# Performance work log

Hardware: AMD Instinct MI355X
Metric: run time of the kernel (lower is better)

Reference implementation:

```python
import jax, jax.numpy as jnp
import numpy as np

N_NODES = 100000
EPS = 1e-5


def _layernorm(x, g, b):
    # per-node layer norm over feature dim
    mu = jnp.mean(x, axis=-1, keepdims=True)
    var = jnp.mean(jnp.square(x - mu), axis=-1, keepdims=True)
    return (x - mu) * jax.lax.rsqrt(var + EPS) * g + b


def _gcn_conv(x, W, b, src, dst, n_nodes):
    # GCNConv: xW, then symmetric-normalized aggregation with self-loops.
    xw = x @ W  # [N, out]
    ones = jnp.ones(src.shape[0], dtype=x.dtype)
    deg = jax.ops.segment_sum(ones, dst, num_segments=n_nodes) + 1.0  # +1 self loop
    dinv = jax.lax.rsqrt(deg)  # [N]
    norm = dinv[src] * dinv[dst]  # [E]
    msg = xw[src] * norm[:, None]  # [E, out]  <- dominant memory traffic
    agg = jax.ops.segment_sum(msg, dst, num_segments=n_nodes)
    agg = agg + xw * (dinv * dinv)[:, None]  # self-loop contribution
    return agg + b


def setup_inputs() -> dict:
    key = jax.random.key(0)
    ks = jax.random.split(key, 16)
    in_c, hid, out_c = 128, 64, 32
    E = 1_600_000
    d = {}
    d['x'] = jax.random.normal(ks[0], (N_NODES, in_c), dtype=jnp.float32)
    d['edge_index'] = jax.random.randint(ks[1], (2, E), 0, N_NODES, dtype=jnp.int64)

    def lin(k, fi, fo):
        s = 1.0 / np.sqrt(fi)
        k1, k2 = jax.random.split(k)
        return (jax.random.uniform(k1, (fi, fo), jnp.float32, -s, s),
                jax.random.uniform(k2, (fo,), jnp.float32, -s, s))

    d['W1'], d['b1'] = lin(ks[2], in_c, hid)
    d['g1'], d['be1'] = jnp.ones((hid,), jnp.float32), jnp.zeros((hid,), jnp.float32)
    d['W2'], d['b2'] = lin(ks[3], hid, 2 * hid)
    d['g2'], d['be2'] = jnp.ones((2 * hid,), jnp.float32), jnp.zeros((2 * hid,), jnp.float32)
    d['W3'], d['b3'] = lin(ks[4], 2 * hid, hid)
    d['g3'], d['be3'] = jnp.ones((hid,), jnp.float32), jnp.zeros((hid,), jnp.float32)
    d['lw1'], d['lb1'] = lin(ks[5], hid, hid // 2)
    d['g4'], d['be4'] = jnp.ones((hid // 2,), jnp.float32), jnp.zeros((hid // 2,), jnp.float32)
    d['lw2'], d['lb2'] = lin(ks[6], hid // 2, out_c)
    return d


def reference(x, edge_index, W1, b1, g1, be1, W2, b2, g2, be2, W3, b3, g3, be3,
              lw1, lb1, g4, be4, lw2, lb2):
    src, dst = edge_index[0], edge_index[1]
    h = _gcn_conv(x, W1, b1, src, dst, N_NODES)
    h = jax.nn.elu(_layernorm(h, g1, be1))
    h = _gcn_conv(h, W2, b2, src, dst, N_NODES)
    h = jax.nn.elu(_layernorm(h, g2, be2))
    h = _gcn_conv(h, W3, b3, src, dst, N_NODES)
    h = jax.nn.elu(_layernorm(h, g3, be3))
    h = h @ lw1 + lb1
    h = jax.nn.elu(_layernorm(h, g4, be4))
    return h @ lw2 + lb2
```

## Files before the change

kernel.cpp:

```cpp
#include <hip/hip_runtime.h>
#include <math.h>

#define N_NODES 100000
#define LN_EPS 1e-5f
#define NBUCK ((N_NODES + 255) / 256)
#define EPB 8192

typedef __attribute__((ext_vector_type(8))) short bf16x8;
typedef __attribute__((ext_vector_type(4))) float f32x4;

__device__ __forceinline__ unsigned short f2bf(float f) {
    unsigned int u = __float_as_uint(f);
    return (unsigned short)((u + 0x7FFFu + ((u >> 16) & 1u)) >> 16);
}
__device__ __forceinline__ float bf2f(unsigned short u) {
    return __uint_as_float(((unsigned int)u) << 16);
}


__global__ void count_edges(const int* __restrict__ dst, int* __restrict__ counts, int E) {
    __shared__ int hist[NBUCK];
    for (int b = threadIdx.x; b < NBUCK; b += 512) hist[b] = 0;
    __syncthreads();
    int e0 = blockIdx.x * EPB;
#pragma unroll 4
    for (int i = 0; i < EPB / 512; ++i) {
        int e = e0 + i * 512 + (int)threadIdx.x;
        if (e < E) atomicAdd(&hist[((unsigned)dst[e]) >> 8], 1);
    }
    __syncthreads();
    for (int b = threadIdx.x; b < NBUCK; b += 512)
        counts[blockIdx.x * NBUCK + b] = hist[b];
}

__global__ void scan_pos(const int* __restrict__ counts, int* __restrict__ pos,
                         int* __restrict__ tot, int nblk) {
    __shared__ int s[512];
    int b = blockIdx.x, i = threadIdx.x;
    int v = (i < nblk) ? counts[i * NBUCK + b] : 0;
    s[i] = v;
    __syncthreads();
    for (int off = 1; off < 512; off <<= 1) {
        int t = (i >= off) ? s[i - off] : 0;
        __syncthreads();
        s[i] += t;
        __syncthreads();
    }
    if (i < nblk) pos[i * NBUCK + b] = s[i] - v;
    if (i == 511) tot[b] = s[511];
}

__global__ void scan_base(const int* __restrict__ tot, int* __restrict__ base, int E) {
    __shared__ int s[512];
    int i = threadIdx.x;
    int v = (i < NBUCK) ? tot[i] : 0;
    s[i] = v;
    __syncthreads();
    for (int off = 1; off < 512; off <<= 1) {
        int t = (i >= off) ? s[i - off] : 0;
        __syncthreads();
        s[i] += t;
        __syncthreads();
    }
    if (i < NBUCK) base[i] = s[i] - v;
    if (i == 0) base[NBUCK] = E;
}

__global__ void place_edges(const int* __restrict__ src, const int* __restrict__ dst,
                            const int* __restrict__ pos, const int* __restrict__ base,
                            unsigned* __restrict__ bucket, int E) {
    __shared__ int lcur[NBUCK];
    for (int b = threadIdx.x; b < NBUCK; b += 512)
        lcur[b] = pos[blockIdx.x * NBUCK + b] + base[b];
    __syncthreads();
    int e0 = blockIdx.x * EPB;
#pragma unroll 4
    for (int i = 0; i < EPB / 512; ++i) {
        int e = e0 + i * 512 + (int)threadIdx.x;
        if (e < E) {
            unsigned d = (unsigned)dst[e];
            unsigned s = (unsigned)src[e];
            int p = atomicAdd(&lcur[d >> 8], 1);
            bucket[p] = ((d & 255u) << 24) | s;
        }
    }
}

__global__ void build_csr_node(const unsigned* __restrict__ bucket, const int* __restrict__ base,
                               int* __restrict__ offsets, float* __restrict__ dinv,
                               int* __restrict__ csr, int E) {
    __shared__ int hist[256];
    __shared__ int cur[256];
    int b = blockIdx.x, t = threadIdx.x;
    int r0 = b << 8;
    hist[t] = 0;
    __syncthreads();
    int s0 = base[b], s1 = base[b + 1];
    for (int e = s0 + t; e < s1; e += 256)
        atomicAdd(&hist[bucket[e] >> 24], 1);
    __syncthreads();
    int deg = hist[t];
    for (int off = 1; off < 256; off <<= 1) {
        int tv = (t >= off) ? hist[t - off] : 0;
        __syncthreads();
        hist[t] += tv;
        __syncthreads();
    }
    int excl = hist[t] - deg;
    int node = r0 + t;
    if (node < N_NODES) {
        offsets[node] = s0 + excl;
        dinv[node] = rsqrtf((float)deg + 1.f);
        cur[t] = s0 + excl;
    }
    if (node == N_NODES - 1) offsets[N_NODES] = E;
    __syncthreads();
    for (int e = s0 + t; e < s1; e += 256) {
        unsigned u = bucket[e];
        int p = atomicAdd(&cur[u >> 24], 1);
        csr[p] = (int)(u & 0xFFFFFFu);
    }
}

template <int K, int OUT, bool LN, bool BIAS, bool AF32, bool OF32, bool SCALED>
__launch_bounds__(256)
__global__ void mfma_gemm(const void* __restrict__ Xv, const float* __restrict__ W,
                          const float* __restrict__ bias, const float* __restrict__ gamma,
                          const float* __restrict__ beta, void* __restrict__ Yv, int n,
                          const float* __restrict__ dinvp) {
    constexpr int T  = OUT / 16;
    constexpr int KP = K + 8;

    __shared__ __align__(16) unsigned short sWT[OUT * KP];
    for (int i = threadIdx.x; i < K * OUT; i += 256) {
        int k = i / OUT, o = i - k * OUT;
        sWT[o * KP + k] = f2bf(W[i]);
    }
    __syncthreads();

    int wv = threadIdx.x >> 6, lane = threadIdx.x & 63;
    int quad = lane >> 4, l16 = lane & 15;
    int m0 = (blockIdx.x * 4 + wv) * 16;
    int rowc = min(m0 + l16, n - 1);

    f32x4 acc[T];
#pragma unroll
    for (int t = 0; t < T; ++t) acc[t] = (f32x4){0.f, 0.f, 0.f, 0.f};

#pragma unroll
    for (int s = 0; s < K / 32; ++s) {
        int koff = s * 32 + quad * 8;
        bf16x8 af;
        if (AF32) {
            const float4* X4 = (const float4*)Xv;
            size_t base = ((size_t)rowc * K + koff) >> 2;
            float4 a0 = X4[base];
            float4 a1 = X4[base + 1];
            af[0] = (short)f2bf(a0.x); af[1] = (short)f2bf(a0.y);
            af[2] = (short)f2bf(a0.z); af[3] = (short)f2bf(a0.w);
            af[4] = (short)f2bf(a1.x); af[5] = (short)f2bf(a1.y);
            af[6] = (short)f2bf(a1.z); af[7] = (short)f2bf(a1.w);
        } else {
            const unsigned short* Xb = (const unsigned short*)Xv;
            af = *(const bf16x8*)(Xb + (size_t)rowc * K + koff);
        }
#pragma unroll
        for (int t = 0; t < T; ++t) {
            const bf16x8 bfrag = *(const bf16x8*)&sWT[(t * 16 + l16) * KP + koff];
            acc[t] = __builtin_amdgcn_mfma_f32_16x16x32_bf16(af, bfrag, acc[t], 0, 0, 0);
        }
    }

    float bj[T], gj[T], btj[T];
#pragma unroll
    for (int t = 0; t < T; ++t) {
        int c = t * 16 + l16;
        bj[t]  = BIAS ? bias[c] : 0.f;
        gj[t]  = LN ? gamma[c] : 1.f;
        btj[t] = LN ? beta[c] : 0.f;
    }

    float* Yf = (float*)Yv;
    unsigned short* Yb = (unsigned short*)Yv;

    if (LN) {
        float s[4] = {0.f, 0.f, 0.f, 0.f}, sq[4] = {0.f, 0.f, 0.f, 0.f};
#pragma unroll
        for (int t = 0; t < T; ++t)
#pragma unroll
            for (int r = 0; r < 4; ++r) {
                float v = acc[t][r] + bj[t];
                s[r] += v;
                sq[r] += v * v;
            }
#pragma unroll
        for (int off = 1; off < 16; off <<= 1)
#pragma unroll
            for (int r = 0; r < 4; ++r) {
                s[r] += __shfl_xor(s[r], off, 64);
                sq[r] += __shfl_xor(sq[r], off, 64);
            }
        float mu[4], rs[4];
#pragma unroll
        for (int r = 0; r < 4; ++r) {
            mu[r] = s[r] / OUT;
            float var = sq[r] / OUT - mu[r] * mu[r];
            rs[r] = rsqrtf(var + LN_EPS);
        }
#pragma unroll
        for (int r = 0; r < 4; ++r) {
            int rowg = m0 + quad * 4 + r;
            if (rowg < n) {
                float dv = SCALED ? dinvp[rowg] : 1.f;
#pragma unroll
                for (int t = 0; t < T; ++t) {
                    float y = (acc[t][r] + bj[t] - mu[r]) * rs[r] * gj[t] + btj[t];
                    y = y > 0.f ? y : expm1f(y);
                    if (SCALED) y *= dv;
                    size_t idx = (size_t)rowg * OUT + t * 16 + l16;
                    if (OF32) Yf[idx] = y; else Yb[idx] = f2bf(y);
                }
            }
        }
    } else {
#pragma unroll
        for (int r = 0; r < 4; ++r) {
            int rowg = m0 + quad * 4 + r;
            if (rowg < n) {
                float dv = SCALED ? dinvp[rowg] : 1.f;
#pragma unroll
                for (int t = 0; t < T; ++t) {
                    float y = acc[t][r] + bj[t];
                    if (SCALED) y *= dv;
                    size_t idx = (size_t)rowg * OUT + t * 16 + l16;
                    if (OF32) Yf[idx] = y; else Yb[idx] = f2bf(y);
                }
            }
        }
    }
}

template <bool LN, bool SCALEOUT>
__global__ void gather_rl(const unsigned short* __restrict__ xs, const int* __restrict__ offsets,
                          const int* __restrict__ csr_src, const float* __restrict__ dinv,
                          const float* __restrict__ bias, const float* __restrict__ gamma,
                          const float* __restrict__ beta, unsigned short* __restrict__ out, int n) {
    int wave = threadIdx.x >> 6;
    int lane = threadIdx.x & 63;
    int node = blockIdx.x * (blockDim.x >> 6) + wave;
    if (node >= n) return;
    int beg = offsets[node], end = offsets[node + 1];

    float a0 = 0.f, a1 = 0.f, a2 = 0.f, a3 = 0.f;
    for (int base = beg; base < end; base += 64) {
        int m = min(64, end - base);
        int myS = (lane < m) ? csr_src[base + lane] : 0;
        int k = 0;
        for (; k + 4 <= m; k += 4) {
            int s0 = __builtin_amdgcn_readlane(myS, k);
            int s1 = __builtin_amdgcn_readlane(myS, k + 1);
            int s2 = __builtin_amdgcn_readlane(myS, k + 2);
            int s3 = __builtin_amdgcn_readlane(myS, k + 3);
            unsigned short v0 = xs[((size_t)s0 << 6) + lane];
            unsigned short v1 = xs[((size_t)s1 << 6) + lane];
            unsigned short v2 = xs[((size_t)s2 << 6) + lane];
            unsigned short v3 = xs[((size_t)s3 << 6) + lane];
            a0 += bf2f(v0);
            a1 += bf2f(v1);
            a2 += bf2f(v2);
            a3 += bf2f(v3);
        }
        for (; k < m; ++k) {
            int s0 = __builtin_amdgcn_readlane(myS, k);
            a0 += bf2f(xs[((size_t)s0 << 6) + lane]);
        }
    }

    float dd = dinv[node];
    float self = bf2f(xs[((size_t)node << 6) + lane]);
    float y = (a0 + a1 + a2 + a3 + self) * dd;

    if (!LN) {
        out[((size_t)node << 6) + lane] = f2bf(y);
        return;
    }
    float yb = y + bias[lane];
    float s = yb, sq = yb * yb;
#pragma unroll
    for (int off = 1; off < 64; off <<= 1) {
        s += __shfl_xor(s, off, 64);
        sq += __shfl_xor(sq, off, 64);
    }
    float mu = s * (1.f / 64.f);
    float var = sq * (1.f / 64.f) - mu * mu;
    float rs = rsqrtf(var + LN_EPS);
    float z = (yb - mu) * rs * gamma[lane] + beta[lane];
    z = z > 0.f ? z : expm1f(z);
    if (SCALEOUT) z *= dd;
    out[((size_t)node << 6) + lane] = f2bf(z);
}

extern "C" void kernel_launch(void* const* d_in, const int* in_sizes, int n_in,
                              void* d_out, int out_size, void* d_ws, size_t ws_size,
                              hipStream_t stream) {
    const float* x  = (const float*)d_in[0];
    const int* ei   = (const int*)d_in[1];
    const float* W1 = (const float*)d_in[2];
    const float* b1 = (const float*)d_in[3];
    const float* g1 = (const float*)d_in[4];
    const float* be1= (const float*)d_in[5];
    const float* W2 = (const float*)d_in[6];
    const float* b2 = (const float*)d_in[7];
    const float* g2 = (const float*)d_in[8];
    const float* be2= (const float*)d_in[9];
    const float* W3 = (const float*)d_in[10];
    const float* b3 = (const float*)d_in[11];
    const float* g3 = (const float*)d_in[12];
    const float* be3= (const float*)d_in[13];
    const float* lw1= (const float*)d_in[14];
    const float* lb1= (const float*)d_in[15];
    const float* g4 = (const float*)d_in[16];
    const float* be4= (const float*)d_in[17];
    const float* lw2= (const float*)d_in[18];
    const float* lb2= (const float*)d_in[19];
    float* out = (float*)d_out;

    const int E = in_sizes[1] / 2;
    const int* src = ei;
    const int* dst = ei + E;
    const int N = N_NODES;

    unsigned short* bufA = (unsigned short*)d_ws;
    unsigned short* bufB = bufA + (size_t)N * 128;
    float* dinv    = (float*)(bufB + (size_t)N * 128);
    int*   offsets = (int*)(dinv + N);
    int*   csr     = offsets + N + 1;
    int*   tot     = csr + E;
    int*   base    = tot + NBUCK;

    auto cdiv = [](long long a, long long b) { return (int)((a + b - 1) / b); };
    const int NBLK = cdiv(E, EPB);

    int* counts = (int*)bufA;
    int* pos    = counts + (size_t)NBLK * NBUCK;
    unsigned* bucket = (unsigned*)bufB;

    const int GB = cdiv(N, 64);

    count_edges<<<NBLK, 512, 0, stream>>>(dst, counts, E);
    scan_pos<<<NBUCK, 512, 0, stream>>>(counts, pos, tot, NBLK);
    scan_base<<<1, 512, 0, stream>>>(tot, base, E);
    place_edges<<<NBLK, 512, 0, stream>>>(src, dst, pos, base, bucket, E);
    build_csr_node<<<NBUCK, 256, 0, stream>>>(bucket, base, offsets, dinv, csr, E);

    mfma_gemm<128, 64, false, false, true, false, true><<<GB, 256, 0, stream>>>(
        x, W1, nullptr, nullptr, nullptr, bufA, N, dinv);
    gather_rl<true, true><<<cdiv(N, 4), 256, 0, stream>>>(bufA, offsets, csr, dinv, b1, g1, be1, bufB, N);

    gather_rl<false, false><<<cdiv(N, 4), 256, 0, stream>>>(bufB, offsets, csr, dinv, nullptr, nullptr, nullptr, bufA, N);
    mfma_gemm<64, 128, true, true, false, false, false><<<GB, 256, 0, stream>>>(
        bufA, W2, b2, g2, be2, bufB, N, nullptr);

    mfma_gemm<128, 64, false, false, false, false, true><<<GB, 256, 0, stream>>>(
        bufB, W3, nullptr, nullptr, nullptr, bufA, N, dinv);
    gather_rl<true, false><<<cdiv(N, 4), 256, 0, stream>>>(bufA, offsets, csr, dinv, b3, g3, be3, bufB, N);

    mfma_gemm<64, 32, true, true, false, false, false><<<GB, 256, 0, stream>>>(
        bufB, lw1, lb1, g4, be4, bufA, N, nullptr);

    mfma_gemm<32, 32, false, true, false, true, false><<<GB, 256, 0, stream>>>(
        bufA, lw2, lb2, nullptr, nullptr, out, N, nullptr);
}
```

Measured before the change: 377.4 us.

## Gather four edges per wave with 8-byte vector loads per lane

The neighbor-gather kernel now splits each wave into four 16-lane groups. Each group handles a different edge, and each lane loads 4 bf16 features as one 8-byte vector. Up to 16 loads are issued before any accumulation to raise memory-level parallelism, then the group partials are combined with cross-lane shuffles. The LayerNorm/ELU epilogue works on 4 features per lane and stores packed 8-byte outputs from one group. The cost is more registers per lane, masked work on short neighbor lists, and extra shuffle reductions.

```diff
diff --git a/kernel.cpp b/kernel.cpp
--- a/kernel.cpp
+++ b/kernel.cpp
@@ -241,63 +241,98 @@
 }
 
 template <bool LN, bool SCALEOUT>
-__global__ void gather_rl(const unsigned short* __restrict__ xs, const int* __restrict__ offsets,
-                          const int* __restrict__ csr_src, const float* __restrict__ dinv,
-                          const float* __restrict__ bias, const float* __restrict__ gamma,
-                          const float* __restrict__ beta, unsigned short* __restrict__ out, int n) {
+__launch_bounds__(256)
+__global__ void gather_p(const unsigned short* __restrict__ xs, const int* __restrict__ offsets,
+                         const int* __restrict__ csr_src, const float* __restrict__ dinv,
+                         const float* __restrict__ bias, const float* __restrict__ gamma,
+                         const float* __restrict__ beta, unsigned short* __restrict__ out, int n) {
     int wave = threadIdx.x >> 6;
     int lane = threadIdx.x & 63;
     int node = blockIdx.x * (blockDim.x >> 6) + wave;
     if (node >= n) return;
     int beg = offsets[node], end = offsets[node + 1];
+    int g  = lane >> 4;
+    int fb = (lane & 15) << 3;
+    const char* xsb = (const char*)xs;
 
     float a0 = 0.f, a1 = 0.f, a2 = 0.f, a3 = 0.f;
     for (int base = beg; base < end; base += 64) {
         int m = min(64, end - base);
         int myS = (lane < m) ? csr_src[base + lane] : 0;
-        int k = 0;
-        for (; k + 4 <= m; k += 4) {
-            int s0 = __builtin_amdgcn_readlane(myS, k);
-            int s1 = __builtin_amdgcn_readlane(myS, k + 1);
-            int s2 = __builtin_amdgcn_readlane(myS, k + 2);
-            int s3 = __builtin_amdgcn_readlane(myS, k + 3);
-            unsigned short v0 = xs[((size_t)s0 << 6) + lane];
-            unsigned short v1 = xs[((size_t)s1 << 6) + lane];
-            unsigned short v2 = xs[((size_t)s2 << 6) + lane];
-            unsigned short v3 = xs[((size_t)s3 << 6) + lane];
-            a0 += bf2f(v0);
-            a1 += bf2f(v1);
-            a2 += bf2f(v2);
-            a3 += bf2f(v3);
-        }
-        for (; k < m; ++k) {
-            int s0 = __builtin_amdgcn_readlane(myS, k);
-            a0 += bf2f(xs[((size_t)s0 << 6) + lane]);
-        }
-    }
+        uint2 B[16];
+        float Wt[16];
+#pragma unroll
+        for (int p = 0; p < 16; ++p) {
+            if (p * 4 < m) {
+                int e = p * 4 + g;
+                int s = __shfl(myS, e, 64);
+                bool ok = e < m;
+                unsigned off = ((unsigned)(ok ? s : 0) << 7) | (unsigned)fb;
+                B[p] = *(const uint2*)(xsb + off);
+                Wt[p] = ok ? 1.f : 0.f;
+            }
+        }
+#pragma unroll
+        for (int p = 0; p < 16; ++p) {
+            if (p * 4 < m) {
+                unsigned lo = B[p].x, hi = B[p].y;
+                float w = Wt[p];
+                a0 += __uint_as_float(lo << 16) * w;
+                a1 += __uint_as_float(lo & 0xFFFF0000u) * w;
+                a2 += __uint_as_float(hi << 16) * w;
+                a3 += __uint_as_float(hi & 0xFFFF0000u) * w;
+            }
+        }
+    }
+    a0 += __shfl_xor(a0, 16, 64); a0 += __shfl_xor(a0, 32, 64);
+    a1 += __shfl_xor(a1, 16, 64); a1 += __shfl_xor(a1, 32, 64);
+    a2 += __shfl_xor(a2, 16, 64); a2 += __shfl_xor(a2, 32, 64);
+    a3 += __shfl_xor(a3, 16, 64); a3 += __shfl_xor(a3, 32, 64);
 
     float dd = dinv[node];
-    float self = bf2f(xs[((size_t)node << 6) + lane]);
-    float y = (a0 + a1 + a2 + a3 + self) * dd;
+    uint2 sru = *(const uint2*)(xsb + ((((unsigned)node) << 7) | (unsigned)fb));
+    float y0 = (a0 + __uint_as_float(sru.x << 16)) * dd;
+    float y1 = (a1 + __uint_as_float(sru.x & 0xFFFF0000u)) * dd;
+    float y2 = (a2 + __uint_as_float(sru.y << 16)) * dd;
+    float y3 = (a3 + __uint_as_float(sru.y & 0xFFFF0000u)) * dd;
+
+    unsigned short* orow = out + (((size_t)node) << 6) + ((lane & 15) << 2);
 
     if (!LN) {
-        out[((size_t)node << 6) + lane] = f2bf(y);
+        if (g == 0) {
+            uint2 o;
+            o.x = (unsigned)f2bf(y0) | ((unsigned)f2bf(y1) << 16);
+            o.y = (unsigned)f2bf(y2) | ((unsigned)f2bf(y3) << 16);
+            *(uint2*)orow = o;
+        }
         return;
     }
-    float yb = y + bias[lane];
-    float s = yb, sq = yb * yb;
-#pragma unroll
-    for (int off = 1; off < 64; off <<= 1) {
+    int c0 = (lane & 15) << 2;
+    float4 bv = *(const float4*)(bias + c0);
+    float4 gv = *(const float4*)(gamma + c0);
+    float4 tv = *(const float4*)(beta + c0);
+    y0 += bv.x; y1 += bv.y; y2 += bv.z; y3 += bv.w;
+    float s = y0 + y1 + y2 + y3;
+    float sq = y0 * y0 + y1 * y1 + y2 * y2 + y3 * y3;
+#pragma unroll
+    for (int off = 1; off < 16; off <<= 1) {
         s += __shfl_xor(s, off, 64);
         sq += __shfl_xor(sq, off, 64);
     }
     float mu = s * (1.f / 64.f);
     float var = sq * (1.f / 64.f) - mu * mu;
     float rs = rsqrtf(var + LN_EPS);
-    float z = (yb - mu) * rs * gamma[lane] + beta[lane];
-    z = z > 0.f ? z : expm1f(z);
-    if (SCALEOUT) z *= dd;
-    out[((size_t)node << 6) + lane] = f2bf(z);
+    float z0 = (y0 - mu) * rs * gv.x + tv.x; z0 = z0 > 0.f ? z0 : expm1f(z0);
+    float z1 = (y1 - mu) * rs * gv.y + tv.y; z1 = z1 > 0.f ? z1 : expm1f(z1);
+    float z2 = (y2 - mu) * rs * gv.z + tv.z; z2 = z2 > 0.f ? z2 : expm1f(z2);
+    float z3 = (y3 - mu) * rs * gv.w + tv.w; z3 = z3 > 0.f ? z3 : expm1f(z3);
+    if (SCALEOUT) { z0 *= dd; z1 *= dd; z2 *= dd; z3 *= dd; }
+    if (g == 0) {
+        uint2 o;
+        o.x = (unsigned)f2bf(z0) | ((unsigned)f2bf(z1) << 16);
+        o.y = (unsigned)f2bf(z2) | ((unsigned)f2bf(z3) << 16);
+        *(uint2*)orow = o;
+    }
 }
 
 extern "C" void kernel_launch(void* const* d_in, const int* in_sizes, int n_in,
@@ -355,15 +390,15 @@
 
     mfma_gemm<128, 64, false, false, true, false, true><<<GB, 256, 0, stream>>>(
         x, W1, nullptr, nullptr, nullptr, bufA, N, dinv);
-    gather_rl<true, true><<<cdiv(N, 4), 256, 0, stream>>>(bufA, offsets, csr, dinv, b1, g1, be1, bufB, N);
-
-    gather_rl<false, false><<<cdiv(N, 4), 256, 0, stream>>>(bufB, offsets, csr, dinv, nullptr, nullptr, nullptr, bufA, N);
+    gather_p<true, true><<<cdiv(N, 4), 256, 0, stream>>>(bufA, offsets, csr, dinv, b1, g1, be1, bufB, N);
+
+    gather_p<false, false><<<cdiv(N, 4), 256, 0, stream>>>(bufB, offsets, csr, dinv, nullptr, nullptr, nullptr, bufA, N);
     mfma_gemm<64, 128, true, true, false, false, false><<<GB, 256, 0, stream>>>(
         bufA, W2, b2, g2, be2, bufB, N, nullptr);
 
     mfma_gemm<128, 64, false, false, false, false, true><<<GB, 256, 0, stream>>>(
         bufB, W3, nullptr, nullptr, nullptr, bufA, N, dinv);
-    gather_rl<true, false><<<cdiv(N, 4), 256, 0, stream>>>(bufA, offsets, csr, dinv, b3, g3, be3, bufB, N);
+    gather_p<true, false><<<cdiv(N, 4), 256, 0, stream>>>(bufA, offsets, csr, dinv, b3, g3, be3, bufB, N);
 
     mfma_gemm<64, 32, true, true, false, false, false><<<GB, 256, 0, stream>>>(
         bufB, lw1, lb1, g4, be4, bufA, N, nullptr);
```

Result: slower. 465.0 us (+23.2%).
